# Performance work log

Measured on AMD Instinct MI355X. Metric: run time of the kernel, lower is better.

## Reference

```python
import jax, jax.numpy as jnp
import numpy as np

N_USERS = 100000
EMBED_DIM = 128
N_EDGES = 640000


def setup_inputs() -> dict:
    key = jax.random.key(0)
    k1, k2, k3, k4, k5, k6 = jax.random.split(key, 6)
    # Xavier-normal-ish scale for embedding table
    emb = jax.random.normal(k1, (N_USERS, EMBED_DIM), dtype=jnp.float32) * 0.02
    s = 1.0 / np.sqrt(EMBED_DIM)
    W_l = jax.random.normal(k2, (EMBED_DIM, EMBED_DIM), dtype=jnp.float32) * s
    b_l = jax.random.normal(k3, (EMBED_DIM,), dtype=jnp.float32) * 0.01
    W_r = jax.random.normal(k4, (EMBED_DIM, EMBED_DIM), dtype=jnp.float32) * s
    src = jax.random.randint(k5, (N_EDGES,), 0, N_USERS, dtype=jnp.int64)
    dst = jax.random.randint(k6, (N_EDGES,), 0, N_USERS, dtype=jnp.int64)
    return {"emb": emb, "W_l": W_l, "b_l": b_l, "W_r": W_r, "src": src, "dst": dst}


def reference(emb, W_l, b_l, W_r, src, dst):
    # GraphSAGE (mean aggr) over the full user embedding table.
    # messages gathered from source nodes: [E, D]
    msgs = emb[src]
    agg = jax.ops.segment_sum(msgs, dst, num_segments=N_USERS)  # [N, D]
    deg = jax.ops.segment_sum(jnp.ones((dst.shape[0],), dtype=emb.dtype), dst,
                              num_segments=N_USERS)
    agg = agg / jnp.maximum(deg, 1.0)[:, None]  # mean over neighbors
    # out = lin_l(mean neighbors) + lin_r(self); bias on lin_l only (PyG SAGEConv)
    out = agg @ W_l.T + b_l + emb @ W_r.T
    # dropout (p=0) and batchnorm (is_norm=False) are identity here
    return out
```

## Files before the change

### kernel.cpp

```cpp
#include <hip/hip_runtime.h>
#include <hip/hip_bf16.h>

#define N_USERS   100000
#define EMBED_DIM 128
#define N_EDGES   640000
#define ZERO_ROW  N_USERS
#define SLOTS     32
#define NWIN      2500
#define GRID_INIT 20000

typedef __bf16 bf16x8 __attribute__((ext_vector_type(8)));
typedef float  f32x4  __attribute__((ext_vector_type(4)));

#define OFF_CURSOR 25600256
#define OFF_PERM   26000384
#define OFF_WLSW   38800384
#define OFF_WRSW   38833152

__device__ __forceinline__ unsigned short f2bf_rne(float f) {
    union { float f; unsigned u; } c; c.f = f;
    unsigned u = c.u + 0x7fffu + ((c.u >> 16) & 1u);
    return (unsigned short)(u >> 16);
}
__device__ __forceinline__ float bf2f_lo(unsigned u) {
    union { float f; unsigned u; } c; c.u = u << 16;
    return c.f;
}
__device__ __forceinline__ float bf2f_hi(unsigned u) {
    union { float f; unsigned u; } c; c.u = u & 0xffff0000u;
    return c.f;
}

__global__ __launch_bounds__(256) void k_init(const float* __restrict__ emb,
                                              const float* __restrict__ Wl,
                                              const float* __restrict__ Wr,
                                              const int* __restrict__ src,
                                              const int* __restrict__ dst,
                                              unsigned short* __restrict__ embb,
                                              int* __restrict__ cursor,
                                              int* __restrict__ perm,
                                              unsigned short* __restrict__ wlsw,
                                              unsigned short* __restrict__ wrsw) {
    int b   = blockIdx.x;
    int tid = threadIdx.x;

    {
        int w = b >> 3;
        int cls = b & 7;
        int e = w * 256 + tid;
        int d = dst[e];
        if (((d >> 4) & 7) == cls) {
            int pos = atomicAdd(&cursor[d], 1);
            if (pos < SLOTS) perm[d * SLOTS + pos] = src[e];
        }
    }

    if (b < 6250) {
        int i = b * 256 + tid;
        if (i < 2048) {
            int li = i & 63;
            int kt = (i >> 6) & 3;
            int jt = i >> 8;
            int row  = jt * 16 + (li & 15);
            int colb = kt * 32 + ((li >> 4) << 3);
            const float4* pl = (const float4*)(Wl + row * 128 + colb);
            const float4* pr = (const float4*)(Wr + row * 128 + colb);
            float4 l0 = pl[0], l1 = pl[1];
            float4 r0 = pr[0], r1 = pr[1];
            int o = i * 8;
            wlsw[o+0] = f2bf_rne(l0.x); wlsw[o+1] = f2bf_rne(l0.y);
            wlsw[o+2] = f2bf_rne(l0.z); wlsw[o+3] = f2bf_rne(l0.w);
            wlsw[o+4] = f2bf_rne(l1.x); wlsw[o+5] = f2bf_rne(l1.y);
            wlsw[o+6] = f2bf_rne(l1.z); wlsw[o+7] = f2bf_rne(l1.w);
            wrsw[o+0] = f2bf_rne(r0.x); wrsw[o+1] = f2bf_rne(r0.y);
            wrsw[o+2] = f2bf_rne(r0.z); wrsw[o+3] = f2bf_rne(r0.w);
            wrsw[o+4] = f2bf_rne(r1.x); wrsw[o+5] = f2bf_rne(r1.y);
            wrsw[o+6] = f2bf_rne(r1.z); wrsw[o+7] = f2bf_rne(r1.w);
        }
        if (i < 16) {
            int4 z = {0, 0, 0, 0};
            ((int4*)(embb + (size_t)ZERO_ROW * EMBED_DIM))[i] = z;
        }
        float4 a = ((const float4*)emb)[i * 2 + 0];
        float4 bb = ((const float4*)emb)[i * 2 + 1];
        int4 p;
        p.x = (int)f2bf_rne(a.x)  | ((int)f2bf_rne(a.y)  << 16);
        p.y = (int)f2bf_rne(a.z)  | ((int)f2bf_rne(a.w)  << 16);
        p.z = (int)f2bf_rne(bb.x) | ((int)f2bf_rne(bb.y) << 16);
        p.w = (int)f2bf_rne(bb.z) | ((int)f2bf_rne(bb.w) << 16);
        ((int4*)embb)[i] = p;
    }
}

#define LDS_S 136
__global__ __launch_bounds__(256) void k_fused(const unsigned short* __restrict__ embb,
                                               const int* __restrict__ cursor,
                                               int* __restrict__ perm,
                                               const unsigned short* __restrict__ wlsw,
                                               const unsigned short* __restrict__ wrsw,
                                               const float* __restrict__ bl,
                                               float* __restrict__ out) {
    __shared__ unsigned short sa[32 * LDS_S];
    __shared__ unsigned short se[32 * LDS_S];
    int tid  = threadIdx.x;
    int wave = tid >> 6;
    int lane = tid & 63;
    int quad = lane >> 4;
    int m    = lane & 15;
    int node0 = blockIdx.x * 32;
    int off   = lane * 2;

    const int4* eslab = (const int4*)(embb + (size_t)node0 * EMBED_DIM);
    int4 ve0 = eslab[tid];
    int4 ve1 = eslab[256 + tid];

    if (tid < 32) {
        int n = node0 + tid;
        int c = cursor[n]; c = c < SLOTS ? c : SLOTS;
        int ce = (c + 3) & ~3;
        for (int k = c; k < ce; k++) perm[n * SLOTS + k] = ZERO_ROW;
    }
    __syncthreads();

    int nb = node0 + wave * 8;
    int cN[8];
#pragma unroll
    for (int r = 0; r < 8; r++) {
        int c = cursor[nb + r];
        cN[r] = c < SLOTS ? c : SLOTS;
    }

    const unsigned short* ep = embb;

#pragma unroll
    for (int p = 0; p < 4; p++) {
        int nA = p * 2, nB = nA + 1;
        const int4* gA = (const int4*)(perm + (nb + nA) * SLOTS);
        const int4* gB = (const int4*)(perm + (nb + nB) * SLOTS);
        int ga = (cN[nA] + 3) >> 2;
        int gb = (cN[nB] + 3) >> 2;
        int gmin = ga < gb ? ga : gb;
        float2 accA = {0.f, 0.f}, accB = {0.f, 0.f};
        int t = 0;
#pragma unroll 2
        for (; t < gmin; t++) {
            int4 ia = gA[t];
            int4 ib = gB[t];
            unsigned a0 = *(const unsigned*)(ep + (size_t)ia.x * EMBED_DIM + off);
            unsigned a1 = *(const unsigned*)(ep + (size_t)ia.y * EMBED_DIM + off);
            unsigned a2 = *(const unsigned*)(ep + (size_t)ia.z * EMBED_DIM + off);
            unsigned a3 = *(const unsigned*)(ep + (size_t)ia.w * EMBED_DIM + off);
            unsigned b0 = *(const unsigned*)(ep + (size_t)ib.x * EMBED_DIM + off);
            unsigned b1 = *(const unsigned*)(ep + (size_t)ib.y * EMBED_DIM + off);
            unsigned b2 = *(const unsigned*)(ep + (size_t)ib.z * EMBED_DIM + off);
            unsigned b3 = *(const unsigned*)(ep + (size_t)ib.w * EMBED_DIM + off);
            accA.x += (bf2f_lo(a0) + bf2f_lo(a1)) + (bf2f_lo(a2) + bf2f_lo(a3));
            accA.y += (bf2f_hi(a0) + bf2f_hi(a1)) + (bf2f_hi(a2) + bf2f_hi(a3));
            accB.x += (bf2f_lo(b0) + bf2f_lo(b1)) + (bf2f_lo(b2) + bf2f_lo(b3));
            accB.y += (bf2f_hi(b0) + bf2f_hi(b1)) + (bf2f_hi(b2) + bf2f_hi(b3));
        }
        for (int ta = t; ta < ga; ta++) {
            int4 ia = gA[ta];
            unsigned a0 = *(const unsigned*)(ep + (size_t)ia.x * EMBED_DIM + off);
            unsigned a1 = *(const unsigned*)(ep + (size_t)ia.y * EMBED_DIM + off);
            unsigned a2 = *(const unsigned*)(ep + (size_t)ia.z * EMBED_DIM + off);
            unsigned a3 = *(const unsigned*)(ep + (size_t)ia.w * EMBED_DIM + off);
            accA.x += (bf2f_lo(a0) + bf2f_lo(a1)) + (bf2f_lo(a2) + bf2f_lo(a3));
            accA.y += (bf2f_hi(a0) + bf2f_hi(a1)) + (bf2f_hi(a2) + bf2f_hi(a3));
        }
        for (int tb = t; tb < gb; tb++) {
            int4 ib = gB[tb];
            unsigned b0 = *(const unsigned*)(ep + (size_t)ib.x * EMBED_DIM + off);
            unsigned b1 = *(const unsigned*)(ep + (size_t)ib.y * EMBED_DIM + off);
            unsigned b2 = *(const unsigned*)(ep + (size_t)ib.z * EMBED_DIM + off);
            unsigned b3 = *(const unsigned*)(ep + (size_t)ib.w * EMBED_DIM + off);
            accB.x += (bf2f_lo(b0) + bf2f_lo(b1)) + (bf2f_lo(b2) + bf2f_lo(b3));
            accB.y += (bf2f_hi(b0) + bf2f_hi(b1)) + (bf2f_hi(b2) + bf2f_hi(b3));
        }
        float invA = (cN[nA] > 0) ? 1.0f / (float)cN[nA] : 0.0f;
        float invB = (cN[nB] > 0) ? 1.0f / (float)cN[nB] : 0.0f;
        unsigned oA = (unsigned)f2bf_rne(accA.x * invA) | ((unsigned)f2bf_rne(accA.y * invA) << 16);
        unsigned oB = (unsigned)f2bf_rne(accB.x * invB) | ((unsigned)f2bf_rne(accB.y * invB) << 16);
        *(unsigned*)(sa + (wave * 8 + nA) * LDS_S + off) = oA;
        *(unsigned*)(sa + (wave * 8 + nB) * LDS_S + off) = oB;
    }

    {
        int g = tid, row = g >> 4, c = g & 15;
        *(int4*)(se + row * LDS_S + c * 8) = ve0;
        g = 256 + tid; row = g >> 4; c = g & 15;
        *(int4*)(se + row * LDS_S + c * 8) = ve1;
    }

    int jt0 = wave * 2;
    bf16x8 wl[2][4], wr[2][4];
#pragma unroll
    for (int jj = 0; jj < 2; jj++) {
#pragma unroll
        for (int kt = 0; kt < 4; kt++) {
            size_t o = (size_t)((((jt0 + jj) * 4 + kt) * 64 + lane)) * 8;
            wl[jj][kt] = *(const bf16x8*)((const __bf16*)wlsw + o);
            wr[jj][kt] = *(const bf16x8*)((const __bf16*)wrsw + o);
        }
    }
    float bias[2];
    bias[0] = bl[(jt0 + 0) * 16 + m];
    bias[1] = bl[(jt0 + 1) * 16 + m];

    __syncthreads();

#pragma unroll
    for (int rt = 0; rt < 2; rt++) {
        bf16x8 af[4], ef[4];
#pragma unroll
        for (int kt = 0; kt < 4; kt++) {
            int o = (rt * 16 + m) * LDS_S + kt * 32 + quad * 8;
            af[kt] = *(const bf16x8*)(sa + o);
            ef[kt] = *(const bf16x8*)(se + o);
        }
        f32x4 acc[2] = {{0.f,0.f,0.f,0.f}, {0.f,0.f,0.f,0.f}};
#pragma unroll
        for (int kt = 0; kt < 4; kt++) {
#pragma unroll
            for (int jj = 0; jj < 2; jj++) {
                acc[jj] = __builtin_amdgcn_mfma_f32_16x16x32_bf16(af[kt], wl[jj][kt], acc[jj], 0, 0, 0);
                acc[jj] = __builtin_amdgcn_mfma_f32_16x16x32_bf16(ef[kt], wr[jj][kt], acc[jj], 0, 0, 0);
            }
        }
#pragma unroll
        for (int jj = 0; jj < 2; jj++) {
#pragma unroll
            for (int r = 0; r < 4; r++) {
                int orow = node0 + rt * 16 + quad * 4 + r;
                out[(size_t)orow * EMBED_DIM + (jt0 + jj) * 16 + m] = acc[jj][r] + bias[jj];
            }
        }
    }
}

extern "C" void kernel_launch(void* const* d_in, const int* in_sizes, int n_in,
                              void* d_out, int out_size, void* d_ws, size_t ws_size,
                              hipStream_t stream) {
    const float* emb = (const float*)d_in[0];
    const float* Wl  = (const float*)d_in[1];
    const float* bl  = (const float*)d_in[2];
    const float* Wr  = (const float*)d_in[3];
    const int*   src = (const int*)d_in[4];
    const int*   dst = (const int*)d_in[5];
    float* out = (float*)d_out;

    char* ws = (char*)d_ws;
    unsigned short* embb   = (unsigned short*)ws;
    int*            cursor = (int*)(ws + OFF_CURSOR);
    int*            perm   = (int*)(ws + OFF_PERM);
    unsigned short* wlsw   = (unsigned short*)(ws + OFF_WLSW);
    unsigned short* wrsw   = (unsigned short*)(ws + OFF_WRSW);

    hipMemsetAsync(ws + OFF_CURSOR, 0, 400000, stream);

    k_init<<<GRID_INIT, 256, 0, stream>>>(emb, Wl, Wr, src, dst, embb, cursor, perm, wlsw, wrsw);
    k_fused<<<3125, 256, 0, stream>>>(embb, cursor, perm, wlsw, wrsw, bl, out);
}
```

Baseline: 181.8 us.

## Gather neighbor embeddings from a scaled FP8 copy and drop perm padding pass

New measurement: 180.6 us. About the same (-0.7%).

```diff
diff --git a/kernel.cpp b/kernel.cpp
--- a/kernel.cpp
+++ b/kernel.cpp
@@ -4,18 +4,18 @@
 #define N_USERS   100000
 #define EMBED_DIM 128
 #define N_EDGES   640000
-#define ZERO_ROW  N_USERS
 #define SLOTS     32
-#define NWIN      2500
 #define GRID_INIT 20000
 
 typedef __bf16 bf16x8 __attribute__((ext_vector_type(8)));
 typedef float  f32x4  __attribute__((ext_vector_type(4)));
-
-#define OFF_CURSOR 25600256
-#define OFF_PERM   26000384
-#define OFF_WLSW   38800384
-#define OFF_WRSW   38833152
+typedef float  f32x2  __attribute__((ext_vector_type(2)));
+
+#define OFF_EMBF8  25600384
+#define OFF_CURSOR 38400512
+#define OFF_PERM   38800512
+#define OFF_WLSW   51600512
+#define OFF_WRSW   51633280
 
 __device__ __forceinline__ unsigned short f2bf_rne(float f) {
     union { float f; unsigned u; } c; c.f = f;
@@ -29,6 +29,51 @@
 __device__ __forceinline__ float bf2f_hi(unsigned u) {
     union { float f; unsigned u; } c; c.u = u & 0xffff0000u;
     return c.f;
+}
+
+__device__ __forceinline__ unsigned char f32_to_fp8_sw(float x) {
+    union { float f; unsigned u; } c; c.f = x;
+    unsigned s = (c.u >> 24) & 0x80u;
+    float a = fabsf(x);
+    if (a >= 448.0f) return (unsigned char)(s | 0x7E);
+    if (a >= 0.015625f) {
+        unsigned m = c.u & 0x7fffffffu;
+        unsigned r = m + 0x7ffffu + ((m >> 20) & 1u);
+        int e32 = (int)(r >> 23) - 127;
+        unsigned man3 = (r >> 20) & 0x7u;
+        int E = e32 + 7;
+        if (E >= 16) return (unsigned char)(s | 0x7E);
+        return (unsigned char)(s | (E << 3) | man3);
+    }
+    int n = (int)rintf(a * 512.0f);
+    if (n >= 8) return (unsigned char)(s | 0x08);
+    return (unsigned char)(s | n);
+}
+__device__ __forceinline__ float fp8_to_f32_sw(unsigned char b) {
+    unsigned s = ((unsigned)b & 0x80u) << 24;
+    unsigned E = (b >> 3) & 0xFu;
+    unsigned m = b & 7u;
+    union { unsigned u; float f; } c;
+    if (E == 0) { c.f = (float)m * 0.001953125f; c.u |= s; return c.f; }
+    c.u = s | ((E + 120u) << 23) | (m << 20);
+    return c.f;
+}
+__device__ __forceinline__ unsigned enc_fp8x2(float x, float y) {
+#if __has_builtin(__builtin_amdgcn_cvt_pk_fp8_f32)
+    return (unsigned)__builtin_amdgcn_cvt_pk_fp8_f32(x, y, 0, false) & 0xffffu;
+#else
+    return (unsigned)f32_to_fp8_sw(x) | ((unsigned)f32_to_fp8_sw(y) << 8);
+#endif
+}
+__device__ __forceinline__ f32x2 dec_fp8x2(unsigned short u) {
+#if __has_builtin(__builtin_amdgcn_cvt_pk_f32_fp8)
+    return __builtin_amdgcn_cvt_pk_f32_fp8((unsigned)u, false);
+#else
+    f32x2 r;
+    r[0] = fp8_to_f32_sw((unsigned char)(u & 0xff));
+    r[1] = fp8_to_f32_sw((unsigned char)(u >> 8));
+    return r;
+#endif
 }
 
 __global__ __launch_bounds__(256) void k_init(const float* __restrict__ emb,
@@ -37,6 +82,7 @@
                                               const int* __restrict__ src,
                                               const int* __restrict__ dst,
                                               unsigned short* __restrict__ embb,
+                                              unsigned char* __restrict__ embf8,
                                               int* __restrict__ cursor,
                                               int* __restrict__ perm,
                                               unsigned short* __restrict__ wlsw,
@@ -51,7 +97,7 @@
         int d = dst[e];
         if (((d >> 4) & 7) == cls) {
             int pos = atomicAdd(&cursor[d], 1);
-            if (pos < SLOTS) perm[d * SLOTS + pos] = src[e];
+            if (pos < SLOTS) perm[d * SLOTS + pos] = src[e] + 1;
         }
     }
 
@@ -79,7 +125,8 @@
         }
         if (i < 16) {
             int4 z = {0, 0, 0, 0};
-            ((int4*)(embb + (size_t)ZERO_ROW * EMBED_DIM))[i] = z;
+            ((int4*)embb)[i] = z;
+            if (i < 8) ((int4*)embf8)[i] = z;
         }
         float4 a = ((const float4*)emb)[i * 2 + 0];
         float4 bb = ((const float4*)emb)[i * 2 + 1];
@@ -88,14 +135,21 @@
         p.y = (int)f2bf_rne(a.z)  | ((int)f2bf_rne(a.w)  << 16);
         p.z = (int)f2bf_rne(bb.x) | ((int)f2bf_rne(bb.y) << 16);
         p.w = (int)f2bf_rne(bb.z) | ((int)f2bf_rne(bb.w) << 16);
-        ((int4*)embb)[i] = p;
+        ((int4*)(embb + EMBED_DIM))[i] = p;
+        uint2 q;
+        q.x = enc_fp8x2(a.x * 16.0f, a.y * 16.0f)
+            | (enc_fp8x2(a.z * 16.0f, a.w * 16.0f) << 16);
+        q.y = enc_fp8x2(bb.x * 16.0f, bb.y * 16.0f)
+            | (enc_fp8x2(bb.z * 16.0f, bb.w * 16.0f) << 16);
+        ((uint2*)(embf8 + EMBED_DIM))[i] = q;
     }
 }
 
 #define LDS_S 136
 __global__ __launch_bounds__(256) void k_fused(const unsigned short* __restrict__ embb,
+                                               const unsigned char* __restrict__ embf8,
                                                const int* __restrict__ cursor,
-                                               int* __restrict__ perm,
+                                               const int* __restrict__ perm,
                                                const unsigned short* __restrict__ wlsw,
                                                const unsigned short* __restrict__ wrsw,
                                                const float* __restrict__ bl,
@@ -110,17 +164,9 @@
     int node0 = blockIdx.x * 32;
     int off   = lane * 2;
 
-    const int4* eslab = (const int4*)(embb + (size_t)node0 * EMBED_DIM);
+    const int4* eslab = (const int4*)(embb + ((size_t)node0 + 1) * EMBED_DIM);
     int4 ve0 = eslab[tid];
     int4 ve1 = eslab[256 + tid];
-
-    if (tid < 32) {
-        int n = node0 + tid;
-        int c = cursor[n]; c = c < SLOTS ? c : SLOTS;
-        int ce = (c + 3) & ~3;
-        for (int k = c; k < ce; k++) perm[n * SLOTS + k] = ZERO_ROW;
-    }
-    __syncthreads();
 
     int nb = node0 + wave * 8;
     int cN[8];
@@ -129,8 +175,6 @@
         int c = cursor[nb + r];
         cN[r] = c < SLOTS ? c : SLOTS;
     }
-
-    const unsigned short* ep = embb;
 
 #pragma unroll
     for (int p = 0; p < 4; p++) {
@@ -146,39 +190,47 @@
         for (; t < gmin; t++) {
             int4 ia = gA[t];
             int4 ib = gB[t];
-            unsigned a0 = *(const unsigned*)(ep + (size_t)ia.x * EMBED_DIM + off);
-            unsigned a1 = *(const unsigned*)(ep + (size_t)ia.y * EMBED_DIM + off);
-            unsigned a2 = *(const unsigned*)(ep + (size_t)ia.z * EMBED_DIM + off);
-            unsigned a3 = *(const unsigned*)(ep + (size_t)ia.w * EMBED_DIM + off);
-            unsigned b0 = *(const unsigned*)(ep + (size_t)ib.x * EMBED_DIM + off);
-            unsigned b1 = *(const unsigned*)(ep + (size_t)ib.y * EMBED_DIM + off);
-            unsigned b2 = *(const unsigned*)(ep + (size_t)ib.z * EMBED_DIM + off);
-            unsigned b3 = *(const unsigned*)(ep + (size_t)ib.w * EMBED_DIM + off);
-            accA.x += (bf2f_lo(a0) + bf2f_lo(a1)) + (bf2f_lo(a2) + bf2f_lo(a3));
-            accA.y += (bf2f_hi(a0) + bf2f_hi(a1)) + (bf2f_hi(a2) + bf2f_hi(a3));
-            accB.x += (bf2f_lo(b0) + bf2f_lo(b1)) + (bf2f_lo(b2) + bf2f_lo(b3));
-            accB.y += (bf2f_hi(b0) + bf2f_hi(b1)) + (bf2f_hi(b2) + bf2f_hi(b3));
+            unsigned short a0 = *(const unsigned short*)(embf8 + (size_t)ia.x * EMBED_DIM + off);
+            unsigned short a1 = *(const unsigned short*)(embf8 + (size_t)ia.y * EMBED_DIM + off);
+            unsigned short a2 = *(const unsigned short*)(embf8 + (size_t)ia.z * EMBED_DIM + off);
+            unsigned short a3 = *(const unsigned short*)(embf8 + (size_t)ia.w * EMBED_DIM + off);
+            unsigned short b0 = *(const unsigned short*)(embf8 + (size_t)ib.x * EMBED_DIM + off);
+            unsigned short b1 = *(const unsigned short*)(embf8 + (size_t)ib.y * EMBED_DIM + off);
+            unsigned short b2 = *(const unsigned short*)(embf8 + (size_t)ib.z * EMBED_DIM + off);
+            unsigned short b3 = *(const unsigned short*)(embf8 + (size_t)ib.w * EMBED_DIM + off);
+            f32x2 fa0 = dec_fp8x2(a0), fa1 = dec_fp8x2(a1);
+            f32x2 fa2 = dec_fp8x2(a2), fa3 = dec_fp8x2(a3);
+            f32x2 fb0 = dec_fp8x2(b0), fb1 = dec_fp8x2(b1);
+            f32x2 fb2 = dec_fp8x2(b2), fb3 = dec_fp8x2(b3);
+            accA.x += (fa0[0] + fa1[0]) + (fa2[0] + fa3[0]);
+            accA.y += (fa0[1] + fa1[1]) + (fa2[1] + fa3[1]);
+            accB.x += (fb0[0] + fb1[0]) + (fb2[0] + fb3[0]);
+            accB.y += (fb0[1] + fb1[1]) + (fb2[1] + fb3[1]);
         }
         for (int ta = t; ta < ga; ta++) {
             int4 ia = gA[ta];
-            unsigned a0 = *(const unsigned*)(ep + (size_t)ia.x * EMBED_DIM + off);
-            unsigned a1 = *(const unsigned*)(ep + (size_t)ia.y * EMBED_DIM + off);
-            unsigned a2 = *(const unsigned*)(ep + (size_t)ia.z * EMBED_DIM + off);
-            unsigned a3 = *(const unsigned*)(ep + (size_t)ia.w * EMBED_DIM + off);
-            accA.x += (bf2f_lo(a0) + bf2f_lo(a1)) + (bf2f_lo(a2) + bf2f_lo(a3));
-            accA.y += (bf2f_hi(a0) + bf2f_hi(a1)) + (bf2f_hi(a2) + bf2f_hi(a3));
+            unsigned short a0 = *(const unsigned short*)(embf8 + (size_t)ia.x * EMBED_DIM + off);
+            unsigned short a1 = *(const unsigned short*)(embf8 + (size_t)ia.y * EMBED_DIM + off);
+            unsigned short a2 = *(const unsigned short*)(embf8 + (size_t)ia.z * EMBED_DIM + off);
+            unsigned short a3 = *(const unsigned short*)(embf8 + (size_t)ia.w * EMBED_DIM + off);
+            f32x2 fa0 = dec_fp8x2(a0), fa1 = dec_fp8x2(a1);
+            f32x2 fa2 = dec_fp8x2(a2), fa3 = dec_fp8x2(a3);
+            accA.x += (fa0[0] + fa1[0]) + (fa2[0] + fa3[0]);
+            accA.y += (fa0[1] + fa1[1]) + (fa2[1] + fa3[1]);
         }
         for (int tb = t; tb < gb; tb++) {
             int4 ib = gB[tb];
-            unsigned b0 = *(const unsigned*)(ep + (size_t)ib.x * EMBED_DIM + off);
-            unsigned b1 = *(const unsigned*)(ep + (size_t)ib.y * EMBED_DIM + off);
-            unsigned b2 = *(const unsigned*)(ep + (size_t)ib.z * EMBED_DIM + off);
-            unsigned b3 = *(const unsigned*)(ep + (size_t)ib.w * EMBED_DIM + off);
-            accB.x += (bf2f_lo(b0) + bf2f_lo(b1)) + (bf2f_lo(b2) + bf2f_lo(b3));
-            accB.y += (bf2f_hi(b0) + bf2f_hi(b1)) + (bf2f_hi(b2) + bf2f_hi(b3));
-        }
-        float invA = (cN[nA] > 0) ? 1.0f / (float)cN[nA] : 0.0f;
-        float invB = (cN[nB] > 0) ? 1.0f / (float)cN[nB] : 0.0f;
+            unsigned short b0 = *(const unsigned short*)(embf8 + (size_t)ib.x * EMBED_DIM + off);
+            unsigned short b1 = *(const unsigned short*)(embf8 + (size_t)ib.y * EMBED_DIM + off);
+            unsigned short b2 = *(const unsigned short*)(embf8 + (size_t)ib.z * EMBED_DIM + off);
+            unsigned short b3 = *(const unsigned short*)(embf8 + (size_t)ib.w * EMBED_DIM + off);
+            f32x2 fb0 = dec_fp8x2(b0), fb1 = dec_fp8x2(b1);
+            f32x2 fb2 = dec_fp8x2(b2), fb3 = dec_fp8x2(b3);
+            accB.x += (fb0[0] + fb1[0]) + (fb2[0] + fb3[0]);
+            accB.y += (fb0[1] + fb1[1]) + (fb2[1] + fb3[1]);
+        }
+        float invA = (cN[nA] > 0) ? 0.0625f / (float)cN[nA] : 0.0f;
+        float invB = (cN[nB] > 0) ? 0.0625f / (float)cN[nB] : 0.0f;
         unsigned oA = (unsigned)f2bf_rne(accA.x * invA) | ((unsigned)f2bf_rne(accA.y * invA) << 16);
         unsigned oB = (unsigned)f2bf_rne(accB.x * invB) | ((unsigned)f2bf_rne(accB.y * invB) << 16);
         *(unsigned*)(sa + (wave * 8 + nA) * LDS_S + off) = oA;
@@ -251,13 +303,15 @@
 
     char* ws = (char*)d_ws;
     unsigned short* embb   = (unsigned short*)ws;
+    unsigned char*  embf8  = (unsigned char*)(ws + OFF_EMBF8);
     int*            cursor = (int*)(ws + OFF_CURSOR);
     int*            perm   = (int*)(ws + OFF_PERM);
     unsigned short* wlsw   = (unsigned short*)(ws + OFF_WLSW);
     unsigned short* wrsw   = (unsigned short*)(ws + OFF_WRSW);
 
-    hipMemsetAsync(ws + OFF_CURSOR, 0, 400000, stream);
-
-    k_init<<<GRID_INIT, 256, 0, stream>>>(emb, Wl, Wr, src, dst, embb, cursor, perm, wlsw, wrsw);
-    k_fused<<<3125, 256, 0, stream>>>(embb, cursor, perm, wlsw, wrsw, bl, out);
-}
+    hipMemsetAsync(ws + OFF_CURSOR, 0, 400000 + 12800000, stream);
+
+    k_init<<<GRID_INIT, 256, 0, stream>>>(emb, Wl, Wr, src, dst, embb, embf8,
+                                          cursor, perm, wlsw, wrsw);
+    k_fused<<<3125, 256, 0, stream>>>(embb, embf8, cursor, perm, wlsw, wrsw, bl, out);
+}
```
